# Optimization experiments

Measured on AMD Instinct MI355X. Metric: run time of the kernel, lower is better.

## Reference

```python
import jax, jax.numpy as jnp
import numpy as np

B, T, I, E, K, J = 4, 4096, 512, 16, 1024, 512

def setup_inputs() -> dict:
    key = jax.random.key(0)
    k1, k2, k3 = jax.random.split(key, 3)
    X = jax.random.normal(k1, (B, T, I), dtype=jnp.float32)
    ind = jax.random.randint(k2, (B, E, K), 0, T, dtype=jnp.int64)
    W = jax.random.normal(k3, (E, I, J), dtype=jnp.float32)
    return {"X": X, "ind": ind, "W": W}

def reference(X, ind, W):
    # X: [B,T,I], ind: [B,E,K] indices into T (per batch), W: [E,I,J]
    b, t, i = X.shape
    offset = (jnp.arange(b, dtype=ind.dtype) * t)[:, None, None]  # [B,1,1]
    X_flat = X.reshape(b * t, i)
    gathered = X_flat[ind + offset]              # [B,E,K,I]
    Y = jnp.einsum('beki,eij->bekj', gathered, W)  # [B,E,K,J]
    return Y
```

## Files before the change

### kernel.cpp

```cpp
#include <hip/hip_runtime.h>

#define B_ 4
#define T_ 4096
#define I_ 512
#define E_ 16
#define K_ 1024
#define J_ 512

typedef unsigned short u16;
typedef unsigned int u32;
typedef __attribute__((ext_vector_type(4))) float floatx4;
typedef __attribute__((ext_vector_type(8))) short short8;
typedef __attribute__((ext_vector_type(4))) u16 u16x4;
typedef __attribute__((ext_vector_type(8))) u16 u16x8;

__device__ __forceinline__ u16 f2bf(float f) {
  unsigned int u = __float_as_uint(f);
  u += 0x7FFFu + ((u >> 16) & 1u);
  return (u16)(u >> 16);
}

__device__ __forceinline__ void gload16(const u16* g, u16* l) {
  __builtin_amdgcn_global_load_lds(
      (const __attribute__((address_space(1))) unsigned int*)(g),
      (__attribute__((address_space(3))) unsigned int*)(l),
      16, 0, 0);
}

__global__ __launch_bounds__(256) void prep(const float* __restrict__ X,
                                            const float* __restrict__ W,
                                            u16* __restrict__ Xb,
                                            u16* __restrict__ Wt) {
  const int tid = threadIdx.x;
  const int blk = blockIdx.x;
  if (blk < 1024) {
    __shared__ u16 tile[64][65];
    const int e  = blk >> 6;
    const int bi = (blk >> 3) & 7;
    const int bj = blk & 7;
    const int i0 = bi * 64, j0 = bj * 64;
#pragma unroll
    for (int p = 0; p < 4; ++p) {
      int r = p * 16 + (tid >> 4);
      int c = (tid & 15) * 4;
      floatx4 v = *(const floatx4*)(W + ((size_t)(e * I_ + i0 + r)) * J_ + j0 + c);
      tile[r][c + 0] = f2bf(v[0]);
      tile[r][c + 1] = f2bf(v[1]);
      tile[r][c + 2] = f2bf(v[2]);
      tile[r][c + 3] = f2bf(v[3]);
    }
    __syncthreads();
#pragma unroll
    for (int p = 0; p < 2; ++p) {
      int j = p * 32 + (tid >> 3);
      int ch = tid & 7;
      u16x8 o;
#pragma unroll
      for (int s = 0; s < 8; ++s) o[s] = tile[ch * 8 + s][j];
      *(u16x8*)(Wt + ((size_t)(e * J_ + j0 + j)) * I_ + i0 + ch * 8) = o;
    }
  } else {
    const int n4 = B_ * T_ * I_ / 4;
    int i = (blk - 1024) * 256 + tid;
    const int stride = 2048 * 256;
    for (; i < n4; i += stride) {
      floatx4 v = ((const floatx4*)X)[i];
      u16x4 o;
      o[0] = f2bf(v[0]); o[1] = f2bf(v[1]); o[2] = f2bf(v[2]); o[3] = f2bf(v[3]);
      ((u16x4*)Xb)[i] = o;
    }
  }
}

__global__ __launch_bounds__(256, 2) void gemm_gather(
    const u16* __restrict__ Xb, const u16* __restrict__ Wt,
    const int* __restrict__ ind, float* __restrict__ Y) {
  __shared__ alignas(16) u16 Asf[256 * 64];
  __shared__ alignas(16) u16 Bsf[128 * 64];

  const int tid = threadIdx.x;
  const int blk = blockIdx.x;
  const int m_t = blk & 3;
  const int n_t = (blk >> 2) & 3;
  const int be  = blk >> 4;
  const int e = be & 15;
  const int b = be >> 4;

  const int lane = tid & 63;
  const int wave = tid >> 6;

  const int lr = lane >> 3;
  const int cg = (lane & 7) ^ lr;

  u32 aoff[8];
#pragma unroll
  for (int q = 0; q < 8; ++q) {
    const int r = wave * 64 + q * 8 + lr;
    const int t = ind[be * K_ + m_t * 256 + r];
    aoff[q] = (u32)(b * T_ + t) * I_ + cg * 8;
  }
  const u16* bbase =
      Wt + ((size_t)(e * J_ + n_t * 128 + wave * 32 + lr)) * I_ + cg * 8;
  u16* ald = Asf + (wave * 64) * 64;
  u16* bld = Bsf + (wave * 32) * 64;

  const int wj = (wave & 1) * 64;
  const int wk = (wave >> 1) * 128;
  const int ml = lane & 15;
  const int quad = lane >> 4;

  floatx4 acc[4][8] = {};

  for (int kk = 0; kk < I_; kk += 64) {
#pragma unroll
    for (int q = 0; q < 8; ++q) gload16(Xb + aoff[q] + kk, ald + q * 512);
#pragma unroll
    for (int q = 0; q < 4; ++q) gload16(bbase + q * 8 * I_ + kk, bld + q * 512);
    __syncthreads();
#pragma unroll
    for (int s = 0; s < 2; ++s) {
      const int c = s * 4 + quad;
      short8 wf[4];
#pragma unroll
      for (int i = 0; i < 4; ++i) {
        const int jr = wj + i * 16 + ml;
        wf[i] = *(const short8*)&Bsf[jr * 64 + ((c ^ (jr & 7)) * 8)];
      }
#pragma unroll
      for (int ik = 0; ik < 8; ++ik) {
        const int kr = wk + ik * 16 + ml;
        const short8 xf = *(const short8*)&Asf[kr * 64 + ((c ^ (kr & 7)) * 8)];
#pragma unroll
        for (int iw = 0; iw < 4; ++iw)
          acc[iw][ik] = __builtin_amdgcn_mfma_f32_16x16x32_bf16(
              wf[iw], xf, acc[iw][ik], 0, 0, 0);
      }
    }
    __syncthreads();
  }

#pragma unroll
  for (int iw = 0; iw < 4; ++iw) {
    const int j0 = n_t * 128 + wj + iw * 16 + quad * 4;
#pragma unroll
    for (int ik = 0; ik < 8; ++ik) {
      const int k0 = m_t * 256 + wk + ik * 16 + ml;
      *(floatx4*)(Y + ((size_t)(be * K_ + k0)) * J_ + j0) = acc[iw][ik];
    }
  }
}

extern "C" void kernel_launch(void* const* d_in, const int* in_sizes, int n_in,
                              void* d_out, int out_size, void* d_ws,
                              size_t ws_size, hipStream_t stream) {
  const float* X  = (const float*)d_in[0];
  const int* ind  = (const int*)d_in[1];
  const float* W  = (const float*)d_in[2];
  float* Y = (float*)d_out;

  u16* Xb = (u16*)d_ws;
  u16* Wt = (u16*)((char*)d_ws + (size_t)B_ * T_ * I_ * 2);

  prep<<<3072, 256, 0, stream>>>(X, W, Xb, Wt);
  gemm_gather<<<1024, 256, 0, stream>>>(Xb, Wt, ind, Y);
}
```

Measured before the change: 206.4 us.

## Double-buffer LDS tiles and enlarge GEMM block to 256x256 with 8 waves

```diff
diff --git a/kernel.cpp b/kernel.cpp
--- a/kernel.cpp
+++ b/kernel.cpp
@@ -72,17 +72,17 @@
   }
 }
 
-__global__ __launch_bounds__(256, 2) void gemm_gather(
+__global__ __launch_bounds__(512, 2) void gemm_gather(
     const u16* __restrict__ Xb, const u16* __restrict__ Wt,
     const int* __restrict__ ind, float* __restrict__ Y) {
-  __shared__ alignas(16) u16 Asf[256 * 64];
-  __shared__ alignas(16) u16 Bsf[128 * 64];
+  __shared__ alignas(16) u16 Asf[2][256 * 64];
+  __shared__ alignas(16) u16 Bsf[2][256 * 64];
 
   const int tid = threadIdx.x;
   const int blk = blockIdx.x;
   const int m_t = blk & 3;
-  const int n_t = (blk >> 2) & 3;
-  const int be  = blk >> 4;
+  const int n_t = (blk >> 2) & 1;
+  const int be  = blk >> 3;
   const int e = be & 15;
   const int b = be >> 4;
 
@@ -92,31 +92,47 @@
   const int lr = lane >> 3;
   const int cg = (lane & 7) ^ lr;
 
-  u32 aoff[8];
+  u32 aoff[4];
 #pragma unroll
-  for (int q = 0; q < 8; ++q) {
-    const int r = wave * 64 + q * 8 + lr;
+  for (int q = 0; q < 4; ++q) {
+    const int r = wave * 32 + q * 8 + lr;
     const int t = ind[be * K_ + m_t * 256 + r];
     aoff[q] = (u32)(b * T_ + t) * I_ + cg * 8;
   }
   const u16* bbase =
-      Wt + ((size_t)(e * J_ + n_t * 128 + wave * 32 + lr)) * I_ + cg * 8;
-  u16* ald = Asf + (wave * 64) * 64;
-  u16* bld = Bsf + (wave * 32) * 64;
+      Wt + ((size_t)(e * J_ + n_t * 256 + wave * 32 + lr)) * I_ + cg * 8;
 
-  const int wj = (wave & 1) * 64;
-  const int wk = (wave >> 1) * 128;
+  const int wj = (wave & 3) * 64;
+  const int wk = (wave >> 2) * 128;
   const int ml = lane & 15;
   const int quad = lane >> 4;
 
   floatx4 acc[4][8] = {};
 
-  for (int kk = 0; kk < I_; kk += 64) {
+  {
+    u16* ald = &Asf[0][wave * 2048];
+    u16* bld = &Bsf[0][wave * 2048];
 #pragma unroll
-    for (int q = 0; q < 8; ++q) gload16(Xb + aoff[q] + kk, ald + q * 512);
+    for (int q = 0; q < 4; ++q) gload16(Xb + aoff[q], ald + q * 512);
 #pragma unroll
-    for (int q = 0; q < 4; ++q) gload16(bbase + q * 8 * I_ + kk, bld + q * 512);
-    __syncthreads();
+    for (int q = 0; q < 4; ++q) gload16(bbase + q * 8 * I_, bld + q * 512);
+  }
+  asm volatile("s_waitcnt vmcnt(0)" ::: "memory");
+  __builtin_amdgcn_s_barrier();
+
+#pragma unroll
+  for (int it = 0; it < 8; ++it) {
+    const int cur = it & 1;
+    const int kk = it * 64;
+    if (it < 7) {
+      u16* ald = &Asf[cur ^ 1][wave * 2048];
+      u16* bld = &Bsf[cur ^ 1][wave * 2048];
+#pragma unroll
+      for (int q = 0; q < 4; ++q) gload16(Xb + aoff[q] + kk + 64, ald + q * 512);
+#pragma unroll
+      for (int q = 0; q < 4; ++q)
+        gload16(bbase + q * 8 * I_ + kk + 64, bld + q * 512);
+    }
 #pragma unroll
     for (int s = 0; s < 2; ++s) {
       const int c = s * 4 + quad;
@@ -124,24 +140,25 @@
 #pragma unroll
       for (int i = 0; i < 4; ++i) {
         const int jr = wj + i * 16 + ml;
-        wf[i] = *(const short8*)&Bsf[jr * 64 + ((c ^ (jr & 7)) * 8)];
+        wf[i] = *(const short8*)&Bsf[cur][jr * 64 + ((c ^ (jr & 7)) * 8)];
       }
 #pragma unroll
       for (int ik = 0; ik < 8; ++ik) {
         const int kr = wk + ik * 16 + ml;
-        const short8 xf = *(const short8*)&Asf[kr * 64 + ((c ^ (kr & 7)) * 8)];
+        const short8 xf = *(const short8*)&Asf[cur][kr * 64 + ((c ^ (kr & 7)) * 8)];
 #pragma unroll
         for (int iw = 0; iw < 4; ++iw)
           acc[iw][ik] = __builtin_amdgcn_mfma_f32_16x16x32_bf16(
               wf[iw], xf, acc[iw][ik], 0, 0, 0);
       }
     }
-    __syncthreads();
+    asm volatile("s_waitcnt vmcnt(0)" ::: "memory");
+    __builtin_amdgcn_s_barrier();
   }
 
 #pragma unroll
   for (int iw = 0; iw < 4; ++iw) {
-    const int j0 = n_t * 128 + wj + iw * 16 + quad * 4;
+    const int j0 = n_t * 256 + wj + iw * 16 + quad * 4;
 #pragma unroll
     for (int ik = 0; ik < 8; ++ik) {
       const int k0 = m_t * 256 + wk + ik * 16 + ml;
@@ -162,5 +179,5 @@
   u16* Wt = (u16*)((char*)d_ws + (size_t)B_ * T_ * I_ * 2);
 
   prep<<<3072, 256, 0, stream>>>(X, W, Xb, Wt);
-  gemm_gather<<<1024, 256, 0, stream>>>(Xb, Wt, ind, Y);
+  gemm_gather<<<512, 512, 0, stream>>>(Xb, Wt, ind, Y);
 }
```

New measurement: 213.2 us. 3.3% more time.

## Double-buffer gathered X tiles in LDS and load W fragments directly to registers

Applied to the files above, without the earlier changes.

```diff
diff --git a/kernel.cpp b/kernel.cpp
--- a/kernel.cpp
+++ b/kernel.cpp
@@ -75,11 +75,10 @@
 __global__ __launch_bounds__(256, 2) void gemm_gather(
     const u16* __restrict__ Xb, const u16* __restrict__ Wt,
     const int* __restrict__ ind, float* __restrict__ Y) {
-  __shared__ alignas(16) u16 Asf[256 * 64];
-  __shared__ alignas(16) u16 Bsf[128 * 64];
+  __shared__ alignas(16) u16 Asf[2][256 * 64];
 
   const int tid = threadIdx.x;
-  const int blk = blockIdx.x;
+  const int blk = ((int)blockIdx.x & 7) * 128 + ((int)blockIdx.x >> 3);
   const int m_t = blk & 3;
   const int n_t = (blk >> 2) & 3;
   const int be  = blk >> 4;
@@ -99,45 +98,72 @@
     const int t = ind[be * K_ + m_t * 256 + r];
     aoff[q] = (u32)(b * T_ + t) * I_ + cg * 8;
   }
-  const u16* bbase =
-      Wt + ((size_t)(e * J_ + n_t * 128 + wave * 32 + lr)) * I_ + cg * 8;
-  u16* ald = Asf + (wave * 64) * 64;
-  u16* bld = Bsf + (wave * 32) * 64;
 
   const int wj = (wave & 1) * 64;
   const int wk = (wave >> 1) * 128;
   const int ml = lane & 15;
   const int quad = lane >> 4;
 
+  const u16* __restrict__ wbase =
+      Wt + ((size_t)(e * J_ + n_t * 128 + wj + ml)) * I_ + quad * 8;
+
   floatx4 acc[4][8] = {};
+  short8 wfA[8], wfB[8];
 
-  for (int kk = 0; kk < I_; kk += 64) {
 #pragma unroll
-    for (int q = 0; q < 8; ++q) gload16(Xb + aoff[q] + kk, ald + q * 512);
+  for (int i = 0; i < 4; ++i) {
+    wfA[i]     = *(const short8*)(wbase + i * 16 * I_);
+    wfA[4 + i] = *(const short8*)(wbase + i * 16 * I_ + 32);
+  }
+  {
+    u16* ald = &Asf[0][wave * 4096];
 #pragma unroll
-    for (int q = 0; q < 4; ++q) gload16(bbase + q * 8 * I_ + kk, bld + q * 512);
-    __syncthreads();
-#pragma unroll
-    for (int s = 0; s < 2; ++s) {
-      const int c = s * 4 + quad;
-      short8 wf[4];
-#pragma unroll
-      for (int i = 0; i < 4; ++i) {
-        const int jr = wj + i * 16 + ml;
-        wf[i] = *(const short8*)&Bsf[jr * 64 + ((c ^ (jr & 7)) * 8)];
-      }
-#pragma unroll
-      for (int ik = 0; ik < 8; ++ik) {
-        const int kr = wk + ik * 16 + ml;
-        const short8 xf = *(const short8*)&Asf[kr * 64 + ((c ^ (kr & 7)) * 8)];
-#pragma unroll
-        for (int iw = 0; iw < 4; ++iw)
-          acc[iw][ik] = __builtin_amdgcn_mfma_f32_16x16x32_bf16(
-              wf[iw], xf, acc[iw][ik], 0, 0, 0);
-      }
-    }
-    __syncthreads();
+    for (int q = 0; q < 8; ++q) gload16(Xb + aoff[q], ald + q * 512);
   }
+  asm volatile("s_waitcnt vmcnt(0)" ::: "memory");
+  __builtin_amdgcn_s_barrier();
+
+#define GSTEP(IT, CURBUF, WCUR, WNXT)                                          \
+  {                                                                            \
+    constexpr int kk = (IT) * 64;                                              \
+    if ((IT) < 7) {                                                            \
+      u16* ald = &Asf[(CURBUF) ^ 1][wave * 4096];                              \
+      _Pragma("unroll")                                                        \
+      for (int q = 0; q < 8; ++q)                                              \
+        gload16(Xb + aoff[q] + kk + 64, ald + q * 512);                        \
+      _Pragma("unroll")                                                        \
+      for (int i = 0; i < 4; ++i) {                                            \
+        WNXT[i]     = *(const short8*)(wbase + i * 16 * I_ + kk + 64);         \
+        WNXT[4 + i] = *(const short8*)(wbase + i * 16 * I_ + 32 + kk + 64);    \
+      }                                                                        \
+    }                                                                          \
+    _Pragma("unroll")                                                          \
+    for (int s = 0; s < 2; ++s) {                                              \
+      const int c = s * 4 + quad;                                              \
+      _Pragma("unroll")                                                        \
+      for (int ik = 0; ik < 8; ++ik) {                                         \
+        const int kr = wk + ik * 16 + ml;                                      \
+        const short8 xf =                                                      \
+            *(const short8*)&Asf[CURBUF][kr * 64 + ((c ^ (kr & 7)) * 8)];      \
+        _Pragma("unroll")                                                      \
+        for (int iw = 0; iw < 4; ++iw)                                         \
+          acc[iw][ik] = __builtin_amdgcn_mfma_f32_16x16x32_bf16(               \
+              WCUR[s * 4 + iw], xf, acc[iw][ik], 0, 0, 0);                     \
+      }                                                                        \
+    }                                                                          \
+    asm volatile("s_waitcnt vmcnt(0)" ::: "memory");                           \
+    __builtin_amdgcn_s_barrier();                                              \
+  }
+
+  GSTEP(0, 0, wfA, wfB)
+  GSTEP(1, 1, wfB, wfA)
+  GSTEP(2, 0, wfA, wfB)
+  GSTEP(3, 1, wfB, wfA)
+  GSTEP(4, 0, wfA, wfB)
+  GSTEP(5, 1, wfB, wfA)
+  GSTEP(6, 0, wfA, wfB)
+  GSTEP(7, 1, wfB, wfA)
+#undef GSTEP
 
 #pragma unroll
   for (int iw = 0; iw < 4; ++iw) {
```

Result: slower. 222.1 us (+7.6%).
